# Performance work log

Measured on AMD Instinct MI355X. Metric: run time of the kernel, lower is better.

The kernel has to match this reference:

```python
import jax, jax.numpy as jnp
import numpy as np

HIDDEN = 2048
NUM_HEADS = 16
HEAD_DIM = HIDDEN // NUM_HEADS  # 128
LATENT = HIDDEN // 8            # 256
ROPE_THETA = 100000.0


def setup_inputs() -> dict:
    key = jax.random.key(0)
    ks = jax.random.split(key, 7)
    s = 0.02
    x = jax.random.normal(ks[0], (4, 1024, HIDDEN), dtype=jnp.float32)
    # weights stored as [in, out] (transpose of torch nn.Linear.weight)
    w_q_down = jax.random.normal(ks[1], (HIDDEN, LATENT), dtype=jnp.float32) * s
    w_kv_down = jax.random.normal(ks[2], (HIDDEN, LATENT), dtype=jnp.float32) * s
    w_q_up = jax.random.normal(ks[3], (LATENT, HIDDEN), dtype=jnp.float32) * s
    w_k_up = jax.random.normal(ks[4], (LATENT, HIDDEN), dtype=jnp.float32) * s
    w_v_up = jax.random.normal(ks[5], (LATENT, HIDDEN), dtype=jnp.float32) * s
    w_o = jax.random.normal(ks[6], (HIDDEN, HIDDEN), dtype=jnp.float32) * s
    return {"x": x, "w_q_down": w_q_down, "w_kv_down": w_kv_down,
            "w_q_up": w_q_up, "w_k_up": w_k_up, "w_v_up": w_v_up, "w_o": w_o}


def _rope_cos_sin(seq_len, dtype):
    # Llama rotary: inv_freq over even dims, emb = concat(freqs, freqs)
    inv_freq = 1.0 / (ROPE_THETA ** (jnp.arange(0, HEAD_DIM, 2, dtype=jnp.float32) / HEAD_DIM))
    pos = jnp.arange(seq_len, dtype=jnp.float32)
    freqs = pos[:, None] * inv_freq[None, :]          # [S, D/2]
    emb = jnp.concatenate([freqs, freqs], axis=-1)    # [S, D]
    return jnp.cos(emb).astype(dtype), jnp.sin(emb).astype(dtype)


def _rotate_half(t):
    h = t.shape[-1] // 2
    return jnp.concatenate([-t[..., h:], t[..., :h]], axis=-1)


def reference(x, w_q_down, w_kv_down, w_q_up, w_k_up, w_v_up, w_o):
    B, S, H = x.shape
    q_latent = x @ w_q_down                 # [B,S,latent]
    kv_latent = x @ w_kv_down               # [B,S,latent]
    q = (q_latent @ w_q_up).reshape(B, S, NUM_HEADS, HEAD_DIM)
    k = (kv_latent @ w_k_up).reshape(B, S, NUM_HEADS, HEAD_DIM)
    v = (kv_latent @ w_v_up).reshape(B, S, NUM_HEADS, HEAD_DIM)

    cos, sin = _rope_cos_sin(S, x.dtype)    # [S,D]
    cos = cos[None, :, None, :]             # [1,S,1,D] (unsqueeze_dim=2)
    sin = sin[None, :, None, :]
    q = q * cos + _rotate_half(q) * sin
    k = k * cos + _rotate_half(k) * sin

    # [B,H,S,D]
    q = q.transpose(0, 2, 1, 3)
    k = k.transpose(0, 2, 1, 3)
    v = v.transpose(0, 2, 1, 3)

    scale = 1.0 / jnp.sqrt(jnp.asarray(HEAD_DIM, dtype=x.dtype))
    scores = jnp.einsum('bhqd,bhkd->bhqk', q, k) * scale
    causal = jnp.tril(jnp.ones((S, S), dtype=bool))
    scores = jnp.where(causal[None, None], scores, jnp.finfo(scores.dtype).min)
    probs = jax.nn.softmax(scores, axis=-1)
    attn = jnp.einsum('bhqk,bhkd->bhqd', probs, v)  # [B,H,S,D]
    attn = attn.transpose(0, 2, 1, 3).reshape(B, S, H)
    return attn @ w_o
```

## Files before the change

### kernel.cpp

```cpp
#include <hip/hip_runtime.h>
#include <hip/hip_bf16.h>

typedef unsigned short u16;
typedef unsigned int u32;
typedef __attribute__((ext_vector_type(8))) __bf16 bf16x8;
typedef __attribute__((ext_vector_type(4))) float f32x4;

#define HID 2048
#define NH 16
#define HD 128
#define LAT 256
#define BATCH 4
#define SEQ 1024

__device__ __forceinline__ u16 f2bf(float f) {
  union { float f; u32 u; } v; v.f = f;
  u32 r = v.u + 0x7fffu + ((v.u >> 16) & 1u);
  return (u16)(r >> 16);
}

typedef const __attribute__((address_space(1))) u32 as1_u32;
typedef __attribute__((address_space(3))) u32 as3_u32;

__device__ __forceinline__ void load_lds16(const void* g, void* l) {
  __builtin_amdgcn_global_load_lds((as1_u32*)g, (as3_u32*)l, 16, 0, 0);
}

template<int WM, int WN, int MR, int NR>
__device__ __forceinline__ void gemm_core(const u16* __restrict__ A, const u16* __restrict__ Bt,
    int K, int lda, int ldb, int arow0, int brow0, u16* As, u16* Bs, f32x4 acc[MR][NR]) {
  constexpr int BM = WM * MR * 16, BN = WN * NR * 16;
  constexpr int NW = WM * WN;
  constexpr int ACH = (BM * 32) / 512;
  constexpr int BCH = (BN * 32) / 512;
  const int tid = threadIdx.x;
  const int lane = tid & 63, wave = tid >> 6;
  const int wm = wave % WM, wn = wave / WM;
  const int fr = lane & 15, fq = lane >> 4;

  for (int kt = 0; kt < K; kt += 32) {
    __syncthreads();
    #pragma unroll
    for (int cc = 0; cc < ACH / NW; ++cc) {
      int c = wave + cc * NW;
      int r = c * 16 + (lane >> 2);
      int col = (lane & 3) * 8;
      load_lds16(&A[(size_t)(arow0 + r) * lda + kt + col], &As[c * 512]);
    }
    #pragma unroll
    for (int cc = 0; cc < BCH / NW; ++cc) {
      int c = wave + cc * NW;
      int r = c * 16 + (lane >> 2);
      int col = (lane & 3) * 8;
      load_lds16(&Bt[(size_t)(brow0 + r) * ldb + kt + col], &Bs[c * 512]);
    }
    asm volatile("s_waitcnt vmcnt(0)" ::: "memory");
    __syncthreads();
    bf16x8 af[MR], bfr[NR];
    #pragma unroll
    for (int m = 0; m < MR; ++m)
      af[m] = *(const bf16x8*)&As[(wm * MR * 16 + m * 16 + fr) * 32 + fq * 8];
    #pragma unroll
    for (int n = 0; n < NR; ++n)
      bfr[n] = *(const bf16x8*)&Bs[(wn * NR * 16 + n * 16 + fr) * 32 + fq * 8];
    #pragma unroll
    for (int m = 0; m < MR; ++m)
      #pragma unroll
      for (int n = 0; n < NR; ++n)
        acc[m][n] = __builtin_amdgcn_mfma_f32_16x16x32_bf16(af[m], bfr[n], acc[m][n], 0, 0, 0);
  }
}

__global__ void __launch_bounds__(256) k_cvt(const float* __restrict__ in, u16* __restrict__ o, int n4) {
  int i = blockIdx.x * blockDim.x + threadIdx.x;
  if (i < n4) {
    float4 v = ((const float4*)in)[i];
    union { u16 s[4]; uint2 u; } w;
    w.s[0] = f2bf(v.x); w.s[1] = f2bf(v.y); w.s[2] = f2bf(v.z); w.s[3] = f2bf(v.w);
    ((uint2*)o)[i] = w.u;
  }
}

__global__ void __launch_bounds__(256) k_transpose3(const float* __restrict__ in0,
    const float* __restrict__ in1, const float* __restrict__ in2,
    u16* __restrict__ o0, u16* __restrict__ o1, u16* __restrict__ o2, int R, int C) {
  __shared__ float t[32][33];
  const float* in = blockIdx.z == 0 ? in0 : (blockIdx.z == 1 ? in1 : in2);
  u16* o = blockIdx.z == 0 ? o0 : (blockIdx.z == 1 ? o1 : o2);
  int bx = blockIdx.x * 32, by = blockIdx.y * 32;
  int tx = threadIdx.x, ty = threadIdx.y;
  #pragma unroll
  for (int i = ty; i < 32; i += 8) t[i][tx] = in[(size_t)(by + i) * C + bx + tx];
  __syncthreads();
  #pragma unroll
  for (int i = ty; i < 32; i += 8) o[(size_t)(bx + i) * R + by + tx] = f2bf(t[tx][i]);
}

__global__ void __launch_bounds__(256) k_cossin(float* __restrict__ cosT, float* __restrict__ sinT) {
  int idx = blockIdx.x * 256 + threadIdx.x;
  int s = idx >> 6, d = idx & 63;
  float inv = powf(100000.0f, -(float)d / 64.0f);
  float a = (float)s * inv;
  cosT[idx] = cosf(a);
  sinT[idx] = sinf(a);
}

__global__ void __launch_bounds__(512, 2) k_down(const u16* __restrict__ xb, const u16* __restrict__ wqdT,
    const u16* __restrict__ wkvdT, u16* __restrict__ ql, u16* __restrict__ kvl) {
  __shared__ __align__(16) u16 As[2][128 * 128];
  __shared__ __align__(16) u16 Bs[2][64 * 128];
  const u16* Bt = blockIdx.z ? wkvdT : wqdT;
  u16* out = blockIdx.z ? kvl : ql;
  const int rb = blockIdx.x * 128, cb = blockIdx.y * 64;
  const int tid = threadIdx.x, lane = tid & 63, wave = tid >> 6;
  const int wm = wave & 3, wn = wave >> 2;
  const int fr = lane & 15, fq = lane >> 4;
  const char* Ab = (const char*)xb;
  const char* Bb = (const char*)Bt;
  f32x4 acc[2][2] = {};

  auto stage = [&](int buf, int s) {
    #pragma unroll
    for (int cc = 0; cc < 4; ++cc) {
      int c = wave * 4 + cc;
      int L = c * 1024 + lane * 16;
      int Ls = L ^ (((L >> 8) & 7) << 4);
      int r = Ls >> 8, colb = Ls & 255;
      load_lds16(Ab + (size_t)(rb + r) * 4096 + s * 256 + colb, (char*)As[buf] + c * 1024);
    }
    #pragma unroll
    for (int cc = 0; cc < 2; ++cc) {
      int c = wave * 2 + cc;
      int L = c * 1024 + lane * 16;
      int Ls = L ^ (((L >> 8) & 7) << 4);
      int r = Ls >> 8, colb = Ls & 255;
      load_lds16(Bb + (size_t)(cb + r) * 4096 + s * 256 + colb, (char*)Bs[buf] + c * 1024);
    }
  };

  stage(0, 0);
  int buf = 0;
  for (int s = 0; s < 16; ++s) {
    if (s + 1 < 16) {
      stage(buf ^ 1, s + 1);
      asm volatile("s_waitcnt vmcnt(6)" ::: "memory");
    } else {
      asm volatile("s_waitcnt vmcnt(0)" ::: "memory");
    }
    asm volatile("s_barrier" ::: "memory");

    #pragma unroll
    for (int kk = 0; kk < 4; ++kk) {
      bf16x8 af[2], bfr[2];
      #pragma unroll
      for (int m = 0; m < 2; ++m) {
        int r = wm * 32 + m * 16 + fr;
        af[m] = *(const bf16x8*)((const char*)As[buf] + ((r * 256 + kk * 64 + fq * 16) ^ ((r & 7) << 4)));
      }
      #pragma unroll
      for (int n = 0; n < 2; ++n) {
        int r = wn * 32 + n * 16 + fr;
        bfr[n] = *(const bf16x8*)((const char*)Bs[buf] + ((r * 256 + kk * 64 + fq * 16) ^ ((r & 7) << 4)));
      }
      #pragma unroll
      for (int m = 0; m < 2; ++m)
        #pragma unroll
        for (int n = 0; n < 2; ++n)
          acc[m][n] = __builtin_amdgcn_mfma_f32_16x16x32_bf16(af[m], bfr[n], acc[m][n], 0, 0, 0);
    }

    asm volatile("s_barrier" ::: "memory");
    buf ^= 1;
  }

  #pragma unroll
  for (int m = 0; m < 2; ++m)
    #pragma unroll
    for (int n = 0; n < 2; ++n)
      #pragma unroll
      for (int i = 0; i < 4; ++i)
        out[(size_t)(rb + wm * 32 + m * 16 + fq * 4 + i) * LAT + cb + wn * 32 + n * 16 + fr] =
            f2bf(acc[m][n][i]);
}

__global__ void __launch_bounds__(256) k_up(const u16* __restrict__ ql, const u16* __restrict__ kvl,
    const u16* __restrict__ wquT, const u16* __restrict__ wkuT, const u16* __restrict__ wvuT,
    u16* __restrict__ q, u16* __restrict__ k, u16* __restrict__ vt,
    const float* __restrict__ cosT, const float* __restrict__ sinT) {
  __shared__ __align__(16) u16 As[128 * 32];
  __shared__ __align__(16) u16 Bs[128 * 32];
  const int mode = blockIdx.z;
  const u16* A = (mode == 0) ? ql : kvl;
  const u16* Bt = (mode == 0) ? wquT : (mode == 1 ? wkuT : wvuT);
  const int rb = blockIdx.x * 128;
  const int h = blockIdx.y;
  f32x4 acc[2][8] = {};
  gemm_core<4, 1, 2, 8>(A, Bt, LAT, LAT, LAT, rb, h * HD, As, Bs, acc);
  const int lane = threadIdx.x & 63, wave = threadIdx.x >> 6;
  const int fr = lane & 15, fq = lane >> 4;
  if (mode == 2) {
    #pragma unroll
    for (int m = 0; m < 2; ++m)
      #pragma unroll
      for (int n = 0; n < 8; ++n)
        #pragma unroll
        for (int i = 0; i < 4; ++i) {
          int row = rb + wave * 32 + m * 16 + fq * 4 + i;
          int b = row >> 10, s = row & 1023;
          int sp = (s & ~63) | (((s >> 4) & 1) << 5) | (((s >> 3) & 1) << 4) |
                   (((s >> 2) & 1) << 3) | (((s >> 5) & 1) << 2) | (s & 3);
          vt[(size_t)((b * NH + h) * HD + n * 16 + fr) * SEQ + sp] = f2bf(acc[m][n][i]);
        }
  } else {
    u16* dst = (mode == 0) ? q : k;
    const float scale = (mode == 0) ? 0.08838834764831845f * 1.4426950408889634f : 1.0f;
    #pragma unroll
    for (int m = 0; m < 2; ++m)
      #pragma unroll
      for (int i = 0; i < 4; ++i) {
        int row = rb + wave * 32 + m * 16 + fq * 4 + i;
        int b = row >> 10, s = row & 1023;
        size_t base = (size_t)((b * NH + h) * SEQ + s) * HD;
        #pragma unroll
        for (int j = 0; j < 4; ++j) {
          int dlo = j * 16 + fr;
          float c = cosT[s * 64 + dlo], sn = sinT[s * 64 + dlo];
          float x1 = acc[m][j][i], x2 = acc[m][j + 4][i];
          dst[base + dlo] = f2bf((x1 * c - x2 * sn) * scale);
          dst[base + dlo + 64] = f2bf((x2 * c + x1 * sn) * scale);
        }
      }
  }
}

__global__ void __launch_bounds__(256, 2) k_attn(const u16* __restrict__ Q, const u16* __restrict__ Kc,
    const u16* __restrict__ Vt, u16* __restrict__ O) {
  __shared__ __align__(16) u16 Ks[2][64 * 128];
  __shared__ __align__(16) u16 Vs[2][128 * 64];
  const int f = blockIdx.x;
  const int j = 7 - ((f >> 5) & 7);
  const int bh = (f & 7) * 8 + ((f >> 3) & 3) + (((f >> 8) & 1) << 2);
  const int h = bh & (NH - 1), b = bh >> 4;
  const int tid = threadIdx.x, lane = tid & 63, wave = tid >> 6;
  const int fr = lane & 15, fq = lane >> 4;
  const int qw = j * 128 + wave * 32;
  const size_t qkb = (size_t)bh * SEQ * HD;
  const char* Kbase = (const char*)Kc + qkb * 2;
  const char* Vbase = (const char*)Vt + (size_t)bh * HD * SEQ * 2;
  const int nkt = 2 * j + 2;

  auto stage = [&](int buf, int kt) {
    #pragma unroll
    for (int cc = 0; cc < 4; ++cc) {
      int c = wave * 4 + cc;
      int L = c * 1024 + lane * 16;
      int Lk = L ^ (((L >> 8) & 7) << 4);
      load_lds16(Kbase + (size_t)kt * 16384 + Lk, (char*)Ks[buf] + c * 1024);
      int Lv = L ^ (((L >> 7) & 7) << 4);
      int rv = Lv >> 7, colb = Lv & 127;
      load_lds16(Vbase + (size_t)rv * (SEQ * 2) + (size_t)kt * 128 + colb, (char*)Vs[buf] + c * 1024);
    }
  };

  bf16x8 ones;
  #pragma unroll
  for (int z = 0; z < 8; ++z) ones[z] = (__bf16)1.0f;

  bf16x8 qf[2][4];
  #pragma unroll
  for (int m = 0; m < 2; ++m)
    #pragma unroll
    for (int c = 0; c < 4; ++c)
      qf[m][c] = *(const bf16x8*)&Q[qkb + (size_t)(qw + m * 16 + fr) * HD + c * 32 + fq * 8];

  f32x4 ao[2][8] = {};
  f32x4 lacc[2] = {};

  stage(0, 0);

  int cur = 0;
  for (int t = 0; t < nkt; ++t) {
    if (t + 1 < nkt) {
      stage(cur ^ 1, t + 1);
      asm volatile("s_waitcnt vmcnt(8)" ::: "memory");
    } else {
      asm volatile("s_waitcnt vmcnt(0)" ::: "memory");
    }
    asm volatile("s_barrier" ::: "memory");

    const int k0 = t * 64;
    if (k0 <= qw + 31) {
      f32x4 sc[2][4] = {};
      __builtin_amdgcn_s_setprio(1);
      #pragma unroll
      for (int c = 0; c < 4; ++c)
        #pragma unroll
        for (int n = 0; n < 4; ++n) {
          int rr = n * 16 + fr;
          int off = (rr * 256 + c * 64 + fq * 16) ^ ((rr & 7) << 4);
          bf16x8 kf = *(const bf16x8*)((const char*)Ks[cur] + off);
          #pragma unroll
          for (int m = 0; m < 2; ++m)
            sc[m][n] = __builtin_amdgcn_mfma_f32_16x16x32_bf16(kf, qf[m][c], sc[m][n], 0, 0, 0);
        }
      __builtin_amdgcn_s_setprio(0);

      bf16x8 pa[2][2];
      #pragma unroll
      for (int m = 0; m < 2; ++m) {
        const bool needmask = (k0 + 63 > qw + m * 16);
        const int qrow = qw + m * 16 + fr;
        float p[4][4];
        #pragma unroll
        for (int n = 0; n < 4; ++n)
          #pragma unroll
          for (int i = 0; i < 4; ++i) {
            float sv = sc[m][n][i];
            if (needmask) {
              int kg = k0 + n * 16 + fq * 4 + i;
              sv = (kg <= qrow) ? sv : -1e30f;
            }
            p[n][i] = exp2f(sv);
          }
        #pragma unroll
        for (int kf = 0; kf < 2; ++kf) {
          union { bf16x8 v; u32 w[4]; } pu;
          asm("v_cvt_pk_bf16_f32 %0, %1, %2" : "=v"(pu.w[0]) : "v"(p[kf][0]), "v"(p[kf][1]));
          asm("v_cvt_pk_bf16_f32 %0, %1, %2" : "=v"(pu.w[1]) : "v"(p[kf][2]), "v"(p[kf][3]));
          asm("v_cvt_pk_bf16_f32 %0, %1, %2" : "=v"(pu.w[2]) : "v"(p[2 + kf][0]), "v"(p[2 + kf][1]));
          asm("v_cvt_pk_bf16_f32 %0, %1, %2" : "=v"(pu.w[3]) : "v"(p[2 + kf][2]), "v"(p[2 + kf][3]));
          pa[m][kf] = pu.v;
        }
      }

      __builtin_amdgcn_s_setprio(1);
      #pragma unroll
      for (int m = 0; m < 2; ++m) {
        lacc[m] = __builtin_amdgcn_mfma_f32_16x16x32_bf16(pa[m][0], ones, lacc[m], 0, 0, 0);
        lacc[m] = __builtin_amdgcn_mfma_f32_16x16x32_bf16(pa[m][1], ones, lacc[m], 0, 0, 0);
      }
      #pragma unroll
      for (int jj = 0; jj < 8; ++jj)
        #pragma unroll
        for (int kf = 0; kf < 2; ++kf) {
          int rv = jj * 16 + fr;
          int off = (rv * 128 + kf * 64 + fq * 16) ^ ((rv & 7) << 4);
          bf16x8 vf = *(const bf16x8*)((const char*)Vs[cur] + off);
          #pragma unroll
          for (int m = 0; m < 2; ++m)
            ao[m][jj] = __builtin_amdgcn_mfma_f32_16x16x32_bf16(pa[m][kf], vf, ao[m][jj], 0, 0, 0);
        }
      __builtin_amdgcn_s_setprio(0);
    }
    asm volatile("s_barrier" ::: "memory");
    cur ^= 1;
  }

  #pragma unroll
  for (int m = 0; m < 2; ++m)
    #pragma unroll
    for (int i = 0; i < 4; ++i) {
      float inv = 1.f / lacc[m][i];
      int s = qw + m * 16 + fq * 4 + i;
      size_t base = (size_t)(b * SEQ + s) * HID + h * HD;
      #pragma unroll
      for (int jj = 0; jj < 8; ++jj)
        O[base + jj * 16 + fr] = f2bf(ao[m][jj][i] * inv);
    }
}

__global__ void __launch_bounds__(256) k_out(const u16* __restrict__ at, const u16* __restrict__ woT,
    float* __restrict__ out) {
  __shared__ __align__(16) u16 As[128 * 128];
  __shared__ __align__(16) u16 Bs[128 * 128];
  const int rb = blockIdx.x * 128, cb = blockIdx.y * 128;
  const int tid = threadIdx.x, lane = tid & 63, wave = tid >> 6;
  const int wm = wave & 1, wn = wave >> 1;
  const int fr = lane & 15, fq = lane >> 4;
  const char* Ab = (const char*)at;
  const char* Bb = (const char*)woT;

  f32x4 acc[4][4] = {};

  for (int kt = 0; kt < HID; kt += 128) {
    __syncthreads();
    #pragma unroll
    for (int cc = 0; cc < 8; ++cc) {
      int c = wave * 8 + cc;
      int L = c * 1024 + lane * 16;
      int Ls = L ^ (((L >> 8) & 7) << 4);
      int r = Ls >> 8, colb = Ls & 255;
      load_lds16(Ab + (size_t)(rb + r) * (HID * 2) + kt * 2 + colb, (char*)As + c * 1024);
      load_lds16(Bb + (size_t)(cb + r) * (HID * 2) + kt * 2 + colb, (char*)Bs + c * 1024);
    }
    asm volatile("s_waitcnt vmcnt(0)" ::: "memory");
    __syncthreads();

    #pragma unroll
    for (int kk = 0; kk < 4; ++kk) {
      bf16x8 af[4], bfr[4];
      #pragma unroll
      for (int m = 0; m < 4; ++m) {
        int r = wm * 64 + m * 16 + fr;
        af[m] = *(const bf16x8*)((const char*)As + ((r * 256 + kk * 64 + fq * 16) ^ ((r & 7) << 4)));
      }
      #pragma unroll
      for (int n = 0; n < 4; ++n) {
        int r = wn * 64 + n * 16 + fr;
        bfr[n] = *(const bf16x8*)((const char*)Bs + ((r * 256 + kk * 64 + fq * 16) ^ ((r & 7) << 4)));
      }
      #pragma unroll
      for (int m = 0; m < 4; ++m)
        #pragma unroll
        for (int n = 0; n < 4; ++n)
          acc[m][n] = __builtin_amdgcn_mfma_f32_16x16x32_bf16(af[m], bfr[n], acc[m][n], 0, 0, 0);
    }
  }

  #pragma unroll
  for (int m = 0; m < 4; ++m)
    #pragma unroll
    for (int n = 0; n < 4; ++n)
      #pragma unroll
      for (int i = 0; i < 4; ++i)
        out[(size_t)(rb + wm * 64 + m * 16 + fq * 4 + i) * HID + cb + wn * 64 + n * 16 + fr] =
            acc[m][n][i];
}

extern "C" void kernel_launch(void* const* d_in, const int* in_sizes, int n_in,
                              void* d_out, int out_size, void* d_ws, size_t ws_size,
                              hipStream_t stream) {
  const float* x    = (const float*)d_in[0];
  const float* wqd  = (const float*)d_in[1];
  const float* wkvd = (const float*)d_in[2];
  const float* wqu  = (const float*)d_in[3];
  const float* wku  = (const float*)d_in[4];
  const float* wvu  = (const float*)d_in[5];
  const float* wo   = (const float*)d_in[6];
  float* out = (float*)d_out;

  char* p = (char*)d_ws;
  u16* xb    = (u16*)(p + 0);
  u16* at    = xb;
  u16* wqdT  = (u16*)(p + 16777216);
  u16* wkvdT = (u16*)(p + 17825792);
  u16* wquT  = (u16*)(p + 18874368);
  u16* wkuT  = (u16*)(p + 19922944);
  u16* wvuT  = (u16*)(p + 20971520);
  u16* woT   = (u16*)(p + 22020096);
  u16* ql    = (u16*)(p + 30408704);
  u16* kvl   = (u16*)(p + 32505856);
  u16* q     = (u16*)(p + 34603008);
  u16* kk    = (u16*)(p + 51380224);
  u16* vt    = (u16*)(p + 68157440);
  float* cosT = (float*)(p + 84934656);
  float* sinT = (float*)(p + 85196800);

  k_cvt<<<8192, 256, 0, stream>>>(x, xb, 2097152);
  k_transpose3<<<dim3(8, 64, 2), dim3(32, 8), 0, stream>>>(wqd, wkvd, wkvd, wqdT, wkvdT, wkvdT, 2048, 256);
  k_transpose3<<<dim3(64, 8, 3), dim3(32, 8), 0, stream>>>(wqu, wku, wvu, wquT, wkuT, wvuT, 256, 2048);
  k_transpose3<<<dim3(64, 64, 1), dim3(32, 8), 0, stream>>>(wo, wo, wo, woT, woT, woT, 2048, 2048);
  k_cossin<<<256, 256, 0, stream>>>(cosT, sinT);

  k_down<<<dim3(32, 4, 2), 512, 0, stream>>>(xb, wqdT, wkvdT, ql, kvl);
  k_up<<<dim3(32, 16, 3), 256, 0, stream>>>(ql, kvl, wquT, wkuT, wvuT, q, kk, vt, cosT, sinT);
  k_attn<<<512, 256, 0, stream>>>(q, kk, vt, at);
  k_out<<<dim3(32, 16), 256, 0, stream>>>(at, woT, out);
}
```

Before: 161.8 us.

## Pair heavy and light causal query tiles in one 16-wave attention block

The attention kernel now runs 1024-thread blocks of 16 waves, with 256 blocks covering 64 batch-heads by 4 tile pairs. Each block pairs query tile j with tile 7-j, so every block does the same amount of causal work and the stage loads from K/V are shared. Each wave now handles 16 query rows instead of 32, which halves per-wave register use but doubles K/V LDS reads per unit of MFMA work. Only one 1024-thread block fits per CU and the barriers span more waves, and waves on the light tile sit idle through the later key tiles.

```diff
diff --git a/kernel.cpp b/kernel.cpp
--- a/kernel.cpp
+++ b/kernel.cpp
@@ -233,48 +233,44 @@
   }
 }
 
-__global__ void __launch_bounds__(256, 2) k_attn(const u16* __restrict__ Q, const u16* __restrict__ Kc,
+__global__ void __launch_bounds__(1024, 1) k_attn(const u16* __restrict__ Q, const u16* __restrict__ Kc,
     const u16* __restrict__ Vt, u16* __restrict__ O) {
   __shared__ __align__(16) u16 Ks[2][64 * 128];
   __shared__ __align__(16) u16 Vs[2][128 * 64];
   const int f = blockIdx.x;
-  const int j = 7 - ((f >> 5) & 7);
-  const int bh = (f & 7) * 8 + ((f >> 3) & 3) + (((f >> 8) & 1) << 2);
+  const int bh = (f & 7) * 8 + ((f >> 3) & 7);
+  const int jp = f >> 6;
+  const int jh = 7 - jp, jl = jp;
   const int h = bh & (NH - 1), b = bh >> 4;
   const int tid = threadIdx.x, lane = tid & 63, wave = tid >> 6;
   const int fr = lane & 15, fq = lane >> 4;
-  const int qw = j * 128 + wave * 32;
+  const int qw = ((wave < 8) ? jh : jl) * 128 + (wave & 7) * 16;
   const size_t qkb = (size_t)bh * SEQ * HD;
   const char* Kbase = (const char*)Kc + qkb * 2;
   const char* Vbase = (const char*)Vt + (size_t)bh * HD * SEQ * 2;
-  const int nkt = 2 * j + 2;
+  const int nkt = 2 * jh + 2;
 
   auto stage = [&](int buf, int kt) {
-    #pragma unroll
-    for (int cc = 0; cc < 4; ++cc) {
-      int c = wave * 4 + cc;
-      int L = c * 1024 + lane * 16;
-      int Lk = L ^ (((L >> 8) & 7) << 4);
-      load_lds16(Kbase + (size_t)kt * 16384 + Lk, (char*)Ks[buf] + c * 1024);
-      int Lv = L ^ (((L >> 7) & 7) << 4);
-      int rv = Lv >> 7, colb = Lv & 127;
-      load_lds16(Vbase + (size_t)rv * (SEQ * 2) + (size_t)kt * 128 + colb, (char*)Vs[buf] + c * 1024);
-    }
+    int c = wave;
+    int L = c * 1024 + lane * 16;
+    int Lk = L ^ (((L >> 8) & 7) << 4);
+    load_lds16(Kbase + (size_t)kt * 16384 + Lk, (char*)Ks[buf] + c * 1024);
+    int Lv = L ^ (((L >> 7) & 7) << 4);
+    int rv = Lv >> 7, colb = Lv & 127;
+    load_lds16(Vbase + (size_t)rv * (SEQ * 2) + (size_t)kt * 128 + colb, (char*)Vs[buf] + c * 1024);
   };
 
   bf16x8 ones;
   #pragma unroll
   for (int z = 0; z < 8; ++z) ones[z] = (__bf16)1.0f;
 
-  bf16x8 qf[2][4];
-  #pragma unroll
-  for (int m = 0; m < 2; ++m)
-    #pragma unroll
-    for (int c = 0; c < 4; ++c)
-      qf[m][c] = *(const bf16x8*)&Q[qkb + (size_t)(qw + m * 16 + fr) * HD + c * 32 + fq * 8];
-
-  f32x4 ao[2][8] = {};
-  f32x4 lacc[2] = {};
+  bf16x8 qf[4];
+  #pragma unroll
+  for (int c = 0; c < 4; ++c)
+    qf[c] = *(const bf16x8*)&Q[qkb + (size_t)(qw + fr) * HD + c * 32 + fq * 8];
+
+  f32x4 ao[8] = {};
+  f32x4 lacc = {};
 
   stage(0, 0);
 
@@ -282,15 +278,15 @@
   for (int t = 0; t < nkt; ++t) {
     if (t + 1 < nkt) {
       stage(cur ^ 1, t + 1);
-      asm volatile("s_waitcnt vmcnt(8)" ::: "memory");
+      asm volatile("s_waitcnt vmcnt(2)" ::: "memory");
     } else {
       asm volatile("s_waitcnt vmcnt(0)" ::: "memory");
     }
     asm volatile("s_barrier" ::: "memory");
 
     const int k0 = t * 64;
-    if (k0 <= qw + 31) {
-      f32x4 sc[2][4] = {};
+    if (k0 <= qw + 15) {
+      f32x4 sc[4] = {};
       __builtin_amdgcn_s_setprio(1);
       #pragma unroll
       for (int c = 0; c < 4; ++c)
@@ -299,46 +295,38 @@
           int rr = n * 16 + fr;
           int off = (rr * 256 + c * 64 + fq * 16) ^ ((rr & 7) << 4);
           bf16x8 kf = *(const bf16x8*)((const char*)Ks[cur] + off);
-          #pragma unroll
-          for (int m = 0; m < 2; ++m)
-            sc[m][n] = __builtin_amdgcn_mfma_f32_16x16x32_bf16(kf, qf[m][c], sc[m][n], 0, 0, 0);
+          sc[n] = __builtin_amdgcn_mfma_f32_16x16x32_bf16(kf, qf[c], sc[n], 0, 0, 0);
         }
       __builtin_amdgcn_s_setprio(0);
 
-      bf16x8 pa[2][2];
-      #pragma unroll
-      for (int m = 0; m < 2; ++m) {
-        const bool needmask = (k0 + 63 > qw + m * 16);
-        const int qrow = qw + m * 16 + fr;
-        float p[4][4];
-        #pragma unroll
-        for (int n = 0; n < 4; ++n)
-          #pragma unroll
-          for (int i = 0; i < 4; ++i) {
-            float sv = sc[m][n][i];
-            if (needmask) {
-              int kg = k0 + n * 16 + fq * 4 + i;
-              sv = (kg <= qrow) ? sv : -1e30f;
-            }
-            p[n][i] = exp2f(sv);
+      const bool needmask = (k0 + 63 > qw);
+      const int qrow = qw + fr;
+      float p[4][4];
+      #pragma unroll
+      for (int n = 0; n < 4; ++n)
+        #pragma unroll
+        for (int i = 0; i < 4; ++i) {
+          float sv = sc[n][i];
+          if (needmask) {
+            int kg = k0 + n * 16 + fq * 4 + i;
+            sv = (kg <= qrow) ? sv : -1e30f;
           }
-        #pragma unroll
-        for (int kf = 0; kf < 2; ++kf) {
-          union { bf16x8 v; u32 w[4]; } pu;
-          asm("v_cvt_pk_bf16_f32 %0, %1, %2" : "=v"(pu.w[0]) : "v"(p[kf][0]), "v"(p[kf][1]));
-          asm("v_cvt_pk_bf16_f32 %0, %1, %2" : "=v"(pu.w[1]) : "v"(p[kf][2]), "v"(p[kf][3]));
-          asm("v_cvt_pk_bf16_f32 %0, %1, %2" : "=v"(pu.w[2]) : "v"(p[2 + kf][0]), "v"(p[2 + kf][1]));
-          asm("v_cvt_pk_bf16_f32 %0, %1, %2" : "=v"(pu.w[3]) : "v"(p[2 + kf][2]), "v"(p[2 + kf][3]));
-          pa[m][kf] = pu.v;
+          p[n][i] = exp2f(sv);
         }
+      bf16x8 pa[2];
+      #pragma unroll
+      for (int kf = 0; kf < 2; ++kf) {
+        union { bf16x8 v; u32 w[4]; } pu;
+        asm("v_cvt_pk_bf16_f32 %0, %1, %2" : "=v"(pu.w[0]) : "v"(p[kf][0]), "v"(p[kf][1]));
+        asm("v_cvt_pk_bf16_f32 %0, %1, %2" : "=v"(pu.w[1]) : "v"(p[kf][2]), "v"(p[kf][3]));
+        asm("v_cvt_pk_bf16_f32 %0, %1, %2" : "=v"(pu.w[2]) : "v"(p[2 + kf][0]), "v"(p[2 + kf][1]));
+        asm("v_cvt_pk_bf16_f32 %0, %1, %2" : "=v"(pu.w[3]) : "v"(p[2 + kf][2]), "v"(p[2 + kf][3]));
+        pa[kf] = pu.v;
       }
 
       __builtin_amdgcn_s_setprio(1);
-      #pragma unroll
-      for (int m = 0; m < 2; ++m) {
-        lacc[m] = __builtin_amdgcn_mfma_f32_16x16x32_bf16(pa[m][0], ones, lacc[m], 0, 0, 0);
-        lacc[m] = __builtin_amdgcn_mfma_f32_16x16x32_bf16(pa[m][1], ones, lacc[m], 0, 0, 0);
-      }
+      lacc = __builtin_amdgcn_mfma_f32_16x16x32_bf16(pa[0], ones, lacc, 0, 0, 0);
+      lacc = __builtin_amdgcn_mfma_f32_16x16x32_bf16(pa[1], ones, lacc, 0, 0, 0);
       #pragma unroll
       for (int jj = 0; jj < 8; ++jj)
         #pragma unroll
@@ -346,9 +334,7 @@
           int rv = jj * 16 + fr;
           int off = (rv * 128 + kf * 64 + fq * 16) ^ ((rv & 7) << 4);
           bf16x8 vf = *(const bf16x8*)((const char*)Vs[cur] + off);
-          #pragma unroll
-          for (int m = 0; m < 2; ++m)
-            ao[m][jj] = __builtin_amdgcn_mfma_f32_16x16x32_bf16(pa[m][kf], vf, ao[m][jj], 0, 0, 0);
+          ao[jj] = __builtin_amdgcn_mfma_f32_16x16x32_bf16(pa[kf], vf, ao[jj], 0, 0, 0);
         }
       __builtin_amdgcn_s_setprio(0);
     }
@@ -357,16 +343,14 @@
   }
 
   #pragma unroll
-  for (int m = 0; m < 2; ++m)
-    #pragma unroll
-    for (int i = 0; i < 4; ++i) {
-      float inv = 1.f / lacc[m][i];
-      int s = qw + m * 16 + fq * 4 + i;
-      size_t base = (size_t)(b * SEQ + s) * HID + h * HD;
-      #pragma unroll
-      for (int jj = 0; jj < 8; ++jj)
-        O[base + jj * 16 + fr] = f2bf(ao[m][jj][i] * inv);
-    }
+  for (int i = 0; i < 4; ++i) {
+    float inv = 1.f / lacc[i];
+    int s = qw + fq * 4 + i;
+    size_t base = (size_t)(b * SEQ + s) * HID + h * HD;
+    #pragma unroll
+    for (int jj = 0; jj < 8; ++jj)
+      O[base + jj * 16 + fr] = f2bf(ao[jj][i] * inv);
+  }
 }
 
 __global__ void __launch_bounds__(256) k_out(const u16* __restrict__ at, const u16* __restrict__ woT,
@@ -464,6 +448,6 @@
 
   k_down<<<dim3(32, 4, 2), 512, 0, stream>>>(xb, wqdT, wkvdT, ql, kvl);
   k_up<<<dim3(32, 16, 3), 256, 0, stream>>>(ql, kvl, wquT, wkuT, wvuT, q, kk, vt, cosT, sinT);
-  k_attn<<<512, 256, 0, stream>>>(q, kk, vt, at);
+  k_attn<<<256, 1024, 0, stream>>>(q, kk, vt, at);
   k_out<<<dim3(32, 16), 256, 0, stream>>>(at, woT, out);
 }
```

Result: faster. 151.2 us, median of 2 (-6.6%).

## Pair causal query tiles and split KV tiles across waves in attention

Applied to the files above, without the earlier changes.

The attention kernel now launches 256 blocks of 1024 threads. Each block handles one long and one short causal query tile together to balance work across blocks. Within each group, waves split the KV tiles by odd/even parity, and the partial outputs and row sums are then reduced through LDS before the final store. This targets load imbalance from the causal mask and raises per-block parallelism. In exchange it adds a cross-wave LDS reduction, extra barriers, and a single-block-per-CU occupancy limit.

```diff
diff --git a/kernel.cpp b/kernel.cpp
--- a/kernel.cpp
+++ b/kernel.cpp
@@ -233,33 +233,34 @@
   }
 }
 
-__global__ void __launch_bounds__(256, 2) k_attn(const u16* __restrict__ Q, const u16* __restrict__ Kc,
+__global__ void __launch_bounds__(1024, 1) k_attn(const u16* __restrict__ Q, const u16* __restrict__ Kc,
     const u16* __restrict__ Vt, u16* __restrict__ O) {
   __shared__ __align__(16) u16 Ks[2][64 * 128];
   __shared__ __align__(16) u16 Vs[2][128 * 64];
   const int f = blockIdx.x;
-  const int j = 7 - ((f >> 5) & 7);
-  const int bh = (f & 7) * 8 + ((f >> 3) & 3) + (((f >> 8) & 1) << 2);
+  const int bh = (f & 7) * 8 + ((f >> 3) & 7);
+  const int jp = f >> 6;
+  const int jh = 7 - jp, jl = jp;
   const int h = bh & (NH - 1), b = bh >> 4;
   const int tid = threadIdx.x, lane = tid & 63, wave = tid >> 6;
   const int fr = lane & 15, fq = lane >> 4;
-  const int qw = j * 128 + wave * 32;
+  const int group = wave >> 3;
+  const int rh = wave & 3;
+  const int parity = (wave >> 2) & 1;
+  const int qw = (group ? jl : jh) * 128 + rh * 32;
   const size_t qkb = (size_t)bh * SEQ * HD;
   const char* Kbase = (const char*)Kc + qkb * 2;
   const char* Vbase = (const char*)Vt + (size_t)bh * HD * SEQ * 2;
-  const int nkt = 2 * j + 2;
+  const int nkt = 2 * jh + 2;
 
   auto stage = [&](int buf, int kt) {
-    #pragma unroll
-    for (int cc = 0; cc < 4; ++cc) {
-      int c = wave * 4 + cc;
-      int L = c * 1024 + lane * 16;
-      int Lk = L ^ (((L >> 8) & 7) << 4);
-      load_lds16(Kbase + (size_t)kt * 16384 + Lk, (char*)Ks[buf] + c * 1024);
-      int Lv = L ^ (((L >> 7) & 7) << 4);
-      int rv = Lv >> 7, colb = Lv & 127;
-      load_lds16(Vbase + (size_t)rv * (SEQ * 2) + (size_t)kt * 128 + colb, (char*)Vs[buf] + c * 1024);
-    }
+    int c = wave;
+    int L = c * 1024 + lane * 16;
+    int Lk = L ^ (((L >> 8) & 7) << 4);
+    load_lds16(Kbase + (size_t)kt * 16384 + Lk, (char*)Ks[buf] + c * 1024);
+    int Lv = L ^ (((L >> 7) & 7) << 4);
+    int rv = Lv >> 7, colb = Lv & 127;
+    load_lds16(Vbase + (size_t)rv * (SEQ * 2) + (size_t)kt * 128 + colb, (char*)Vs[buf] + c * 1024);
   };
 
   bf16x8 ones;
@@ -282,14 +283,14 @@
   for (int t = 0; t < nkt; ++t) {
     if (t + 1 < nkt) {
       stage(cur ^ 1, t + 1);
-      asm volatile("s_waitcnt vmcnt(8)" ::: "memory");
+      asm volatile("s_waitcnt vmcnt(2)" ::: "memory");
     } else {
       asm volatile("s_waitcnt vmcnt(0)" ::: "memory");
     }
     asm volatile("s_barrier" ::: "memory");
 
     const int k0 = t * 64;
-    if (k0 <= qw + 31) {
+    if (((t & 1) == parity) && (k0 <= qw + 31)) {
       f32x4 sc[2][4] = {};
       __builtin_amdgcn_s_setprio(1);
       #pragma unroll
@@ -356,17 +357,52 @@
     cur ^= 1;
   }
 
-  #pragma unroll
-  for (int m = 0; m < 2; ++m)
-    #pragma unroll
-    for (int i = 0; i < 4; ++i) {
-      float inv = 1.f / lacc[m][i];
-      int s = qw + m * 16 + fq * 4 + i;
-      size_t base = (size_t)(b * SEQ + s) * HID + h * HD;
-      #pragma unroll
-      for (int jj = 0; jj < 8; ++jj)
-        O[base + jj * 16 + fr] = f2bf(ao[m][jj][i] * inv);
-    }
+  float* cbA = (float*)Ks;
+  float* cbB = (float*)Vs;
+  const int widx = group * 4 + rh;
+  __syncthreads();
+  #pragma unroll
+  for (int m = 0; m < 2; ++m) {
+    if (parity == 1) {
+      #pragma unroll
+      for (int jj = 0; jj < 4; ++jj) {
+        *(f32x4*)&cbA[((widx * 4 + jj) * 64 + lane) * 4] = ao[m][jj];
+        *(f32x4*)&cbB[((widx * 4 + jj) * 64 + lane) * 4] = ao[m][jj + 4];
+      }
+    }
+    __syncthreads();
+    if (parity == 0) {
+      #pragma unroll
+      for (int jj = 0; jj < 4; ++jj) {
+        f32x4 a = *(const f32x4*)&cbA[((widx * 4 + jj) * 64 + lane) * 4];
+        f32x4 v = *(const f32x4*)&cbB[((widx * 4 + jj) * 64 + lane) * 4];
+        ao[m][jj] += a;
+        ao[m][jj + 4] += v;
+      }
+    }
+    __syncthreads();
+  }
+  if (parity == 1) {
+    *(f32x4*)&cbA[(widx * 64 + lane) * 4] = lacc[0];
+    *(f32x4*)&cbB[(widx * 64 + lane) * 4] = lacc[1];
+  }
+  __syncthreads();
+  if (parity == 0) {
+    lacc[0] += *(const f32x4*)&cbA[(widx * 64 + lane) * 4];
+    lacc[1] += *(const f32x4*)&cbB[(widx * 64 + lane) * 4];
+
+    #pragma unroll
+    for (int m = 0; m < 2; ++m)
+      #pragma unroll
+      for (int i = 0; i < 4; ++i) {
+        float inv = 1.f / lacc[m][i];
+        int s = qw + m * 16 + fq * 4 + i;
+        size_t base = (size_t)(b * SEQ + s) * HID + h * HD;
+        #pragma unroll
+        for (int jj = 0; jj < 8; ++jj)
+          O[base + jj * 16 + fr] = f2bf(ao[m][jj][i] * inv);
+      }
+  }
 }
 
 __global__ void __launch_bounds__(256) k_out(const u16* __restrict__ at, const u16* __restrict__ woT,
@@ -464,6 +500,6 @@
 
   k_down<<<dim3(32, 4, 2), 512, 0, stream>>>(xb, wqdT, wkvdT, ql, kvl);
   k_up<<<dim3(32, 16, 3), 256, 0, stream>>>(ql, kvl, wquT, wkuT, wvuT, q, kk, vt, cosT, sinT);
-  k_attn<<<512, 256, 0, stream>>>(q, kk, vt, at);
+  k_attn<<<256, 1024, 0, stream>>>(q, kk, vt, at);
   k_out<<<dim3(32, 16), 256, 0, stream>>>(at, woT, out);
 }
```

Result: slower. 333.3 us (+105.9%).
